# Kernel optimization log

Hardware: AMD Instinct MI355X
Metric: run time of the kernel (lower is better)

## Reference

```python
import jax, jax.numpy as jnp
import numpy as np

N_NODES = 50000
N_EDGES = 800000
IN_F = 128
HID = 64
H1 = 4  # heads layer 1
H2 = 1  # heads layer 2
N_GRAPHS = 32
NEG_SLOPE = 0.2  # PyG GATConv default leaky_relu slope


def _glorot(key, shape):
    fan_in, fan_out = shape[0], shape[-1]
    scale = jnp.sqrt(6.0 / (fan_in + fan_out))
    return jax.random.uniform(key, shape, jnp.float32, -scale, scale)


def setup_inputs() -> dict:
    key = jax.random.key(0)
    ks = jax.random.split(key, 10)
    x = jax.random.normal(ks[0], (N_NODES, IN_F), jnp.float32)
    edge_index = jax.random.randint(ks[1], (2, N_EDGES), 0, N_NODES, jnp.int64)
    batch = jnp.sort(jax.random.randint(ks[2], (N_NODES,), 0, N_GRAPHS, jnp.int64))
    # GATConv layer 1: in 128 -> 4 heads x 64, concat
    W1 = _glorot(ks[3], (IN_F, H1 * HID))
    a_src1 = _glorot(ks[4], (H1, HID))
    a_dst1 = _glorot(ks[5], (H1, HID))
    b1 = jnp.zeros((H1 * HID,), jnp.float32)
    # GATConv layer 2: in 256 -> 1 head x 64
    W2 = _glorot(ks[6], (H1 * HID, H2 * HID))
    a_src2 = _glorot(ks[7], (H2, HID))
    a_dst2 = _glorot(ks[8], (H2, HID))
    b2 = jnp.zeros((H2 * HID,), jnp.float32)
    return {"x": x, "edge_index": edge_index, "batch": batch,
            "W1": W1, "a_src1": a_src1, "a_dst1": a_dst1, "b1": b1,
            "W2": W2, "a_src2": a_src2, "a_dst2": a_dst2, "b2": b2}


def gat_layer(x, src, dst, W, a_src, a_dst, bias, num_nodes):
    """PyG-style GATConv with concat=True output [N, H*C]."""
    H, C = a_src.shape
    h = (x @ W).reshape(num_nodes, H, C)            # [N,H,C]
    alpha_src = jnp.sum(h * a_src[None], axis=-1)   # [N,H]
    alpha_dst = jnp.sum(h * a_dst[None], axis=-1)   # [N,H]
    e = jax.nn.leaky_relu(alpha_src[src] + alpha_dst[dst], NEG_SLOPE)  # [E,H]
    # segment softmax over destination neighborhoods
    m = jax.ops.segment_max(e, dst, num_segments=num_nodes)
    ex = jnp.exp(e - m[dst])
    denom = jax.ops.segment_sum(ex, dst, num_segments=num_nodes)
    alpha = ex / (denom[dst] + 1e-16)               # [E,H]
    out = jax.ops.segment_sum(h[src] * alpha[:, :, None], dst, num_segments=num_nodes)
    return out.reshape(num_nodes, H * C) + bias


def reference(x, edge_index, batch, W1, a_src1, a_dst1, b1, W2, a_src2, a_dst2, b2):
    N = x.shape[0]
    # PyG GATConv adds self-loops by default
    loops = jnp.arange(N, dtype=edge_index.dtype)
    src = jnp.concatenate([edge_index[0], loops])
    dst = jnp.concatenate([edge_index[1], loops])
    h = jax.nn.relu(gat_layer(x, src, dst, W1, a_src1, a_dst1, b1, N))
    h = gat_layer(h, src, dst, W2, a_src2, a_dst2, b2, N)
    # role == 'global': global mean pool over batch ids
    sums = jax.ops.segment_sum(h, batch, num_segments=N_GRAPHS)
    cnt = jax.ops.segment_sum(jnp.ones((N, 1), h.dtype), batch, num_segments=N_GRAPHS)
    return sums / jnp.maximum(cnt, 1.0)
```

## Files before the change

kernel.cpp:

```cpp
#include <hip/hip_runtime.h>
#include <cmath>

#define HID 64
typedef unsigned short ushort_t;
typedef __attribute__((ext_vector_type(8))) short bf16x8;
typedef __attribute__((ext_vector_type(4))) float f32x4;

__device__ inline ushort_t f2b(float f) {
    unsigned u = __float_as_uint(f);
    unsigned r = (u + 0x7fffu + ((u >> 16) & 1u)) >> 16;
    return (ushort_t)r;
}
__device__ inline float b2f(ushort_t b) { return __uint_as_float(((unsigned)b) << 16); }


__global__ void fill_i32(int* __restrict__ p, int v, long n) {
    long i = (long)blockIdx.x * blockDim.x + threadIdx.x;
    long stride = (long)gridDim.x * blockDim.x;
    for (; i < n; i += stride) p[i] = v;
}

__global__ __launch_bounds__(256) void prep_k(const float* __restrict__ W1,
                                              const float* __restrict__ W2,
                                              ushort_t* __restrict__ W1t,
                                              ushort_t* __restrict__ W2t,
                                              const int* __restrict__ batch,
                                              int* __restrict__ cnt_i,
                                              float* __restrict__ outp,
                                              const int* __restrict__ ei,
                                              int* __restrict__ deg,
                                              int N, int E, int NHB) {
    int b = blockIdx.x;
    int t = threadIdx.x;
    if (b < 128) {
        W1t[(size_t)t * 128 + b] = f2b(W1[(size_t)b * 256 + t]);
    } else if (b < 384) {
        int k = b - 128;
        if (t < 64) W2t[(size_t)t * 256 + k] = f2b(W2[(size_t)k * 64 + t]);
    } else if (b == 384) {
        int i = t * 8;
        #pragma unroll
        for (int j = 0; j < 8; ++j) outp[i + j] = 0.f;
    } else if (b < 385 + NHB) {
        __shared__ int lh[32];
        if (t < 32) lh[t] = 0;
        __syncthreads();
        int i = (b - 385) * 256 + t;
        if (i < N) atomicAdd(&lh[batch[i]], 1);
        __syncthreads();
        if (t < 32 && lh[t] > 0) atomicAdd(&cnt_i[t], lh[t]);
    } else {
        int e = (b - 385 - NHB) * 256 + t;
        int T = E + N;
        if (e < T) {
            int d = (e < E) ? ei[E + e] : (e - E);
            atomicAdd(&deg[d], 1);
        }
    }
}


__global__ __launch_bounds__(256) void scan1_k(const int* __restrict__ deg,
                                               int* __restrict__ bsum, int N) {
    int i = blockIdx.x * 256 + threadIdx.x;
    int v = (i < N) ? deg[i] : 0;
    #pragma unroll
    for (int off = 32; off > 0; off >>= 1) v += __shfl_xor(v, off, 64);
    __shared__ int ws[4];
    if ((threadIdx.x & 63) == 0) ws[threadIdx.x >> 6] = v;
    __syncthreads();
    if (threadIdx.x == 0) bsum[blockIdx.x] = ws[0] + ws[1] + ws[2] + ws[3];
}

__global__ __launch_bounds__(256) void scan3_k(const int* __restrict__ deg,
                                               const int* __restrict__ bsum,
                                               int* __restrict__ rowstart, int N, int NB) {
    int t = threadIdx.x;
    int lane = t & 63, wave = t >> 6;
    int pv = (t < NB && t < (int)blockIdx.x) ? bsum[t] : 0;
    #pragma unroll
    for (int off = 32; off > 0; off >>= 1) pv += __shfl_xor(pv, off, 64);
    __shared__ int wsp[4];
    if (lane == 0) wsp[wave] = pv;
    __syncthreads();
    int base = wsp[0] + wsp[1] + wsp[2] + wsp[3];

    int i = blockIdx.x * 256 + t;
    int v = (i < N) ? deg[i] : 0;
    int inc = v;
    #pragma unroll
    for (int off = 1; off < 64; off <<= 1) {
        int u = __shfl_up(inc, off, 64);
        if (lane >= off) inc += u;
    }
    __shared__ int wsum[4];
    if (lane == 63) wsum[wave] = inc;
    __syncthreads();
    int woff = base;
    for (int w = 0; w < wave; ++w) woff += wsum[w];
    int excl = inc - v + woff;
    if (i < N) rowstart[i] = excl;
    if (i == N - 1) rowstart[N] = excl + v;
}

__global__ __launch_bounds__(256) void mega1_k(
        const float* __restrict__ x, const ushort_t* __restrict__ Bt,
        ushort_t* __restrict__ Cb, const float* __restrict__ a_src,
        const float* __restrict__ a_dst, float* __restrict__ os,
        float* __restrict__ od, int M, int NG1,
        const int* __restrict__ ei, int E, int N,
        const int* __restrict__ rowstart, int* __restrict__ cursor,
        int* __restrict__ srcs) {
    __shared__ ushort_t Alds[64][40];
    __shared__ ushort_t Blds[256][40];
    const int tid = threadIdx.x;

    if (blockIdx.x >= NG1) {
        int e = (blockIdx.x - NG1) * 256 + tid;
        int T = E + N;
        if (e < T) {
            int s, d;
            if (e < E) { s = ei[e]; d = ei[E + e]; } else { s = e - E; d = s; }
            int p = atomicAdd(&cursor[d], 1);
            srcs[rowstart[d] + p] = s;
        }
        return;
    }

    const int bm = blockIdx.x * 64;
    const int w = tid >> 6;
    const int l = tid & 63;
    const int lr = l >> 4;
    const int lc = l & 15;
    const int col0 = w * 64;

    f32x4 acc[4][4] = {};

    for (int kk = 0; kk < 4; ++kk) {
        __syncthreads();
        {
            int row = tid >> 2, part = tid & 3;
            int gm = bm + row;
            bf16x8 v = {0, 0, 0, 0, 0, 0, 0, 0};
            if (gm < M) {
                const float* ap = x + (size_t)gm * 128 + kk * 32 + part * 8;
                float4 v0 = *(const float4*)ap;
                float4 v1 = *(const float4*)(ap + 4);
                v[0] = (short)f2b(v0.x); v[1] = (short)f2b(v0.y);
                v[2] = (short)f2b(v0.z); v[3] = (short)f2b(v0.w);
                v[4] = (short)f2b(v1.x); v[5] = (short)f2b(v1.y);
                v[6] = (short)f2b(v1.z); v[7] = (short)f2b(v1.w);
            }
            *(bf16x8*)&Alds[row][part * 8] = v;
        }
        #pragma unroll
        for (int it = 0; it < 4; ++it) {
            int u = tid + it * 256;
            int col = u >> 2, part = u & 3;
            *(bf16x8*)&Blds[col][part * 8] =
                *(const bf16x8*)&Bt[(size_t)col * 128 + kk * 32 + part * 8];
        }
        __syncthreads();

        bf16x8 af[4], bfr[4];
        #pragma unroll
        for (int fr = 0; fr < 4; ++fr)
            af[fr] = *(const bf16x8*)&Alds[fr * 16 + lc][lr * 8];
        #pragma unroll
        for (int fc = 0; fc < 4; ++fc)
            bfr[fc] = *(const bf16x8*)&Blds[col0 + fc * 16 + lc][lr * 8];
        #pragma unroll
        for (int fr = 0; fr < 4; ++fr)
            #pragma unroll
            for (int fc = 0; fc < 4; ++fc)
                acc[fr][fc] = __builtin_amdgcn_mfma_f32_16x16x32_bf16(
                    af[fr], bfr[fc], acc[fr][fc], 0, 0, 0);
    }

    #pragma unroll
    for (int fr = 0; fr < 4; ++fr)
        #pragma unroll
        for (int r = 0; r < 4; ++r) {
            int gm = bm + fr * 16 + lr * 4 + r;
            if (gm >= M) continue;
            #pragma unroll
            for (int fc = 0; fc < 4; ++fc)
                Cb[(size_t)gm * 256 + col0 + fc * 16 + lc] = f2b(acc[fr][fc][r]);
        }

    {
        const int head = w;
        const float* __restrict__ asv = a_src + head * 64;
        const float* __restrict__ adv = a_dst + head * 64;
        #pragma unroll
        for (int fr = 0; fr < 4; ++fr)
            #pragma unroll
            for (int r = 0; r < 4; ++r) {
                float ps = 0.f, pd = 0.f;
                #pragma unroll
                for (int fc = 0; fc < 4; ++fc) {
                    float av = acc[fr][fc][r];
                    ps = fmaf(av, asv[fc * 16 + lc], ps);
                    pd = fmaf(av, adv[fc * 16 + lc], pd);
                }
                #pragma unroll
                for (int off = 1; off < 16; off <<= 1) {
                    ps += __shfl_xor(ps, off, 64);
                    pd += __shfl_xor(pd, off, 64);
                }
                int gm = bm + fr * 16 + lr * 4 + r;
                if (lc == 0 && gm < M) {
                    os[(size_t)gm * 4 + head] = ps;
                    od[(size_t)gm * 4 + head] = pd;
                }
            }
    }
}

template<int WM, int WN, int K, bool B_WHOLE, int AH>
__global__ __launch_bounds__(WM * WN * 64) void gemm_mfma(
        const ushort_t* __restrict__ Ap, const ushort_t* __restrict__ Bt,
        ushort_t* __restrict__ Cb, const float* __restrict__ a_src,
        const float* __restrict__ a_dst, float* __restrict__ os,
        float* __restrict__ od, int M) {
    constexpr int T = WM * WN * 64;
    constexpr int BM = WM * 64;
    constexpr int BN = WN * 64;
    constexpr int BSTR = B_WHOLE ? (K + 8) : 40;

    __shared__ ushort_t Alds[BM][40];
    __shared__ ushort_t Blds[BN][BSTR];

    const int tid = threadIdx.x;
    const int bm = blockIdx.x * BM;
    const int w = tid >> 6;
    const int l = tid & 63;
    const int lr = l >> 4;
    const int lc = l & 15;
    const int row0 = (WM == 1) ? 0 : w * 64;
    const int col0 = (WN == 1) ? 0 : w * 64;

    f32x4 acc[4][4] = {};

    if (B_WHOLE) {
        constexpr int UPR = K / 8;
        for (int u = tid; u < BN * UPR; u += T) {
            int row = u / UPR, j = u % UPR;
            *(bf16x8*)&Blds[row][j * 8] = *(const bf16x8*)&Bt[(size_t)row * K + j * 8];
        }
    }

    for (int kk = 0; kk < K / 32; ++kk) {
        __syncthreads();
        for (int u = tid; u < BM * 4; u += T) {
            int row = u >> 2, part = u & 3;
            int gm = bm + row;
            bf16x8 v = {0, 0, 0, 0, 0, 0, 0, 0};
            if (gm < M)
                v = *(const bf16x8*)(Ap + (size_t)gm * K + kk * 32 + part * 8);
            *(bf16x8*)&Alds[row][part * 8] = v;
        }
        if (!B_WHOLE) {
            for (int u = tid; u < BN * 4; u += T) {
                int col = u >> 2, part = u & 3;
                *(bf16x8*)&Blds[col][part * 8] =
                    *(const bf16x8*)&Bt[(size_t)col * K + kk * 32 + part * 8];
            }
        }
        __syncthreads();

        const int koff = B_WHOLE ? kk * 32 : 0;
        bf16x8 af[4], bfr[4];
        #pragma unroll
        for (int fr = 0; fr < 4; ++fr)
            af[fr] = *(const bf16x8*)&Alds[row0 + fr * 16 + lc][lr * 8];
        #pragma unroll
        for (int fc = 0; fc < 4; ++fc)
            bfr[fc] = *(const bf16x8*)&Blds[col0 + fc * 16 + lc][koff + lr * 8];
        #pragma unroll
        for (int fr = 0; fr < 4; ++fr)
            #pragma unroll
            for (int fc = 0; fc < 4; ++fc)
                acc[fr][fc] = __builtin_amdgcn_mfma_f32_16x16x32_bf16(
                    af[fr], bfr[fc], acc[fr][fc], 0, 0, 0);
    }

    #pragma unroll
    for (int fr = 0; fr < 4; ++fr)
        #pragma unroll
        for (int r = 0; r < 4; ++r) {
            int gm = bm + row0 + fr * 16 + lr * 4 + r;
            if (gm >= M) continue;
            #pragma unroll
            for (int fc = 0; fc < 4; ++fc)
                Cb[(size_t)gm * BN + col0 + fc * 16 + lc] = f2b(acc[fr][fc][r]);
        }

    if (AH > 0) {
        const int head = (WN > 1) ? w : 0;
        const float* __restrict__ asv = a_src + head * 64;
        const float* __restrict__ adv = a_dst + head * 64;
        #pragma unroll
        for (int fr = 0; fr < 4; ++fr)
            #pragma unroll
            for (int r = 0; r < 4; ++r) {
                float ps = 0.f, pd = 0.f;
                #pragma unroll
                for (int fc = 0; fc < 4; ++fc) {
                    float av = acc[fr][fc][r];
                    ps = fmaf(av, asv[fc * 16 + lc], ps);
                    pd = fmaf(av, adv[fc * 16 + lc], pd);
                }
                #pragma unroll
                for (int off = 1; off < 16; off <<= 1) {
                    ps += __shfl_xor(ps, off, 64);
                    pd += __shfl_xor(pd, off, 64);
                }
                int gm = bm + row0 + fr * 16 + lr * 4 + r;
                if (lc == 0 && gm < M) {
                    os[(size_t)gm * AH + head] = ps;
                    od[(size_t)gm * AH + head] = pd;
                }
            }
    }
}

#define MAXD 128
__global__ __launch_bounds__(256) void gat_agg4(const ushort_t* __restrict__ hb,
        const int* __restrict__ rowstart, const int* __restrict__ srcs,
        const float* __restrict__ as, const float* __restrict__ ad,
        const float* __restrict__ bias, ushort_t* __restrict__ outb, int N) {
    __shared__ int ssrc_s[4][MAXD];
    __shared__ float sw_s[4][MAXD][4];
    __shared__ float hstat_s[4][2][4];
    const int wave = threadIdx.x >> 6;
    const int lane = threadIdx.x & 63;
    int d = blockIdx.x * 4 + wave;
    if (d >= N) return;
    int* ssrc = ssrc_s[wave];
    float (*sw)[4] = sw_s[wave];
    int beg = rowstart[d];
    int deg = rowstart[d + 1] - beg;
    int dcap = deg < MAXD ? deg : MAXD;
    for (int i = lane; i < dcap; i += 64) ssrc[i] = srcs[beg + i];

    const int isub = lane >> 2;
    const int hd = lane & 3;
    float adv = ad[d * 4 + hd];
    float vmax = -INFINITY;
    for (int e0 = 0; e0 < deg; e0 += 16) {
        int e = e0 + isub;
        if (e < deg) {
            int s = (e < MAXD) ? ssrc[e] : srcs[beg + e];
            float v = as[s * 4 + hd] + adv;
            v = v > 0.f ? v : 0.2f * v;
            if (e < MAXD) sw[e][hd] = v;
            vmax = fmaxf(vmax, v);
        }
    }
    #pragma unroll
    for (int off = 4; off < 64; off <<= 1) vmax = fmaxf(vmax, __shfl_xor(vmax, off, 64));
    float dsum = 0.f;
    for (int e0 = 0; e0 < deg; e0 += 16) {
        int e = e0 + isub;
        if (e < deg) {
            float v;
            if (e < MAXD) v = sw[e][hd];
            else {
                int s = srcs[beg + e];
                v = as[s * 4 + hd] + adv;
                v = v > 0.f ? v : 0.2f * v;
            }
            float ex = __expf(v - vmax);
            if (e < MAXD) sw[e][hd] = ex;
            dsum += ex;
        }
    }
    #pragma unroll
    for (int off = 4; off < 64; off <<= 1) dsum += __shfl_xor(dsum, off, 64);
    float rden = 1.f / (dsum + 1e-16f);
    for (int e0 = 0; e0 < dcap; e0 += 16) {
        int e = e0 + isub;
        if (e < dcap) sw[e][hd] *= rden;
    }
    if (deg > MAXD && isub == 0) {
        hstat_s[wave][0][hd] = vmax;
        hstat_s[wave][1][hd] = rden;
    }

    const int hd2 = lane >> 4;
    const ushort_t* __restrict__ hrow = hb + (size_t)(lane * 4);
    float a0 = 0.f, a1 = 0.f, a2 = 0.f, a3 = 0.f;
    int e = 0;
    for (; e + 4 <= dcap; e += 4) {
        int s0 = __builtin_amdgcn_readfirstlane(ssrc[e]);
        int s1 = __builtin_amdgcn_readfirstlane(ssrc[e + 1]);
        int s2 = __builtin_amdgcn_readfirstlane(ssrc[e + 2]);
        int s3 = __builtin_amdgcn_readfirstlane(ssrc[e + 3]);
        ushort4 g0 = *(const ushort4*)(hrow + (size_t)s0 * 256);
        ushort4 g1 = *(const ushort4*)(hrow + (size_t)s1 * 256);
        ushort4 g2 = *(const ushort4*)(hrow + (size_t)s2 * 256);
        ushort4 g3 = *(const ushort4*)(hrow + (size_t)s3 * 256);
        float w0 = sw[e][hd2], w1 = sw[e + 1][hd2];
        float w2 = sw[e + 2][hd2], w3 = sw[e + 3][hd2];
        a0 = fmaf(b2f(g0.x), w0, a0); a1 = fmaf(b2f(g0.y), w0, a1);
        a2 = fmaf(b2f(g0.z), w0, a2); a3 = fmaf(b2f(g0.w), w0, a3);
        a0 = fmaf(b2f(g1.x), w1, a0); a1 = fmaf(b2f(g1.y), w1, a1);
        a2 = fmaf(b2f(g1.z), w1, a2); a3 = fmaf(b2f(g1.w), w1, a3);
        a0 = fmaf(b2f(g2.x), w2, a0); a1 = fmaf(b2f(g2.y), w2, a1);
        a2 = fmaf(b2f(g2.z), w2, a2); a3 = fmaf(b2f(g2.w), w2, a3);
        a0 = fmaf(b2f(g3.x), w3, a0); a1 = fmaf(b2f(g3.y), w3, a1);
        a2 = fmaf(b2f(g3.z), w3, a2); a3 = fmaf(b2f(g3.w), w3, a3);
    }
    for (; e < dcap; ++e) {
        int s = __builtin_amdgcn_readfirstlane(ssrc[e]);
        float w = sw[e][hd2];
        ushort4 g = *(const ushort4*)(hrow + (size_t)s * 256);
        a0 = fmaf(b2f(g.x), w, a0); a1 = fmaf(b2f(g.y), w, a1);
        a2 = fmaf(b2f(g.z), w, a2); a3 = fmaf(b2f(g.w), w, a3);
    }
    if (deg > MAXD) {
        float vm2 = hstat_s[wave][0][hd2];
        float rd2 = hstat_s[wave][1][hd2];
        float adv2 = ad[d * 4 + hd2];
        for (int j = MAXD; j < deg; ++j) {
            int s = srcs[beg + j];
            float v = as[s * 4 + hd2] + adv2;
            v = v > 0.f ? v : 0.2f * v;
            float w = __expf(v - vm2) * rd2;
            ushort4 g = *(const ushort4*)(hrow + (size_t)s * 256);
            a0 = fmaf(b2f(g.x), w, a0); a1 = fmaf(b2f(g.y), w, a1);
            a2 = fmaf(b2f(g.z), w, a2); a3 = fmaf(b2f(g.w), w, a3);
        }
    }
    int cb = lane * 4;
    ushort4 ov;
    ov.x = f2b(fmaxf(a0 + bias[cb + 0], 0.f));
    ov.y = f2b(fmaxf(a1 + bias[cb + 1], 0.f));
    ov.z = f2b(fmaxf(a2 + bias[cb + 2], 0.f));
    ov.w = f2b(fmaxf(a3 + bias[cb + 3], 0.f));
    *(ushort4*)&outb[(size_t)d * 256 + cb] = ov;
}

__global__ __launch_bounds__(256) void gat_agg1(const ushort_t* __restrict__ hb,
        const int* __restrict__ rowstart, const int* __restrict__ srcs,
        const float* __restrict__ as, const float* __restrict__ ad,
        const float* __restrict__ bias, const int* __restrict__ batch,
        const int* __restrict__ cnt_i, float* __restrict__ outp, int N) {
    __shared__ int ssrc_s[4][MAXD];
    __shared__ float sw_s[4][MAXD];
    __shared__ float prow[4][64];
    __shared__ int gws[4];
    const int wave = threadIdx.x >> 6;
    const int lane = threadIdx.x & 63;
    int d = blockIdx.x * 4 + wave;
    bool active = d < N;
    if (active) {
        int* ssrc = ssrc_s[wave];
        float* sw = sw_s[wave];
        int beg = rowstart[d];
        int deg = rowstart[d + 1] - beg;
        int dcap = deg < MAXD ? deg : MAXD;
        for (int i = lane; i < dcap; i += 64) ssrc[i] = srcs[beg + i];

        float adv = ad[d];
        float vmax = -INFINITY;
        for (int e0 = 0; e0 < deg; e0 += 64) {
            int e = e0 + lane;
            if (e < deg) {
                int s = (e < MAXD) ? ssrc[e] : srcs[beg + e];
                float v = as[s] + adv;
                v = v > 0.f ? v : 0.2f * v;
                if (e < MAXD) sw[e] = v;
                vmax = fmaxf(vmax, v);
            }
        }
        #pragma unroll
        for (int off = 1; off < 64; off <<= 1) vmax = fmaxf(vmax, __shfl_xor(vmax, off, 64));
        float dsum = 0.f;
        for (int e0 = 0; e0 < deg; e0 += 64) {
            int e = e0 + lane;
            if (e < deg) {
                float v;
                if (e < MAXD) v = sw[e];
                else {
                    int s = srcs[beg + e];
                    v = as[s] + adv;
                    v = v > 0.f ? v : 0.2f * v;
                }
                float ex = __expf(v - vmax);
                if (e < MAXD) sw[e] = ex;
                dsum += ex;
            }
        }
        #pragma unroll
        for (int off = 1; off < 64; off <<= 1) dsum += __shfl_xor(dsum, off, 64);
        float rden = 1.f / (dsum + 1e-16f);
        for (int e0 = 0; e0 < dcap; e0 += 64) {
            int e = e0 + lane;
            if (e < dcap) sw[e] *= rden;
        }

        const int esub = lane >> 4;
        const int cg = lane & 15;
        const ushort_t* __restrict__ hrow = hb + (size_t)(cg * 4);
        float a0 = 0.f, a1 = 0.f, a2 = 0.f, a3 = 0.f;
        int e0 = 0;
        for (; e0 + 8 <= dcap; e0 += 8) {
            int eA = e0 + esub, eB = e0 + esub + 4;
            int sA = ssrc[eA], sB = ssrc[eB];
            float wA = sw[eA], wB = sw[eB];
            ushort4 gA = *(const ushort4*)(hrow + (size_t)sA * 64);
            ushort4 gB = *(const ushort4*)(hrow + (size_t)sB * 64);
            a0 = fmaf(b2f(gA.x), wA, a0); a1 = fmaf(b2f(gA.y), wA, a1);
            a2 = fmaf(b2f(gA.z), wA, a2); a3 = fmaf(b2f(gA.w), wA, a3);
            a0 = fmaf(b2f(gB.x), wB, a0); a1 = fmaf(b2f(gB.y), wB, a1);
            a2 = fmaf(b2f(gB.z), wB, a2); a3 = fmaf(b2f(gB.w), wB, a3);
        }
        for (; e0 < dcap; e0 += 4) {
            int e = e0 + esub;
            if (e < dcap) {
                int s = ssrc[e];
                float w = sw[e];
                ushort4 g = *(const ushort4*)(hrow + (size_t)s * 64);
                a0 = fmaf(b2f(g.x), w, a0); a1 = fmaf(b2f(g.y), w, a1);
                a2 = fmaf(b2f(g.z), w, a2); a3 = fmaf(b2f(g.w), w, a3);
            }
        }
        for (int j = MAXD + esub; j < deg; j += 4) {
            int s = srcs[beg + j];
            float v = as[s] + adv;
            v = v > 0.f ? v : 0.2f * v;
            float w = __expf(v - vmax) * rden;
            ushort4 g = *(const ushort4*)(hrow + (size_t)s * 64);
            a0 = fmaf(b2f(g.x), w, a0); a1 = fmaf(b2f(g.y), w, a1);
            a2 = fmaf(b2f(g.z), w, a2); a3 = fmaf(b2f(g.w), w, a3);
        }
        a0 += __shfl_xor(a0, 16, 64); a0 += __shfl_xor(a0, 32, 64);
        a1 += __shfl_xor(a1, 16, 64); a1 += __shfl_xor(a1, 32, 64);
        a2 += __shfl_xor(a2, 16, 64); a2 += __shfl_xor(a2, 32, 64);
        a3 += __shfl_xor(a3, 16, 64); a3 += __shfl_xor(a3, 32, 64);
        int g = batch[d];
        if (esub == 0) {
            float cntf = fmaxf((float)cnt_i[g], 1.f);
            float rc = 1.f / cntf;
            int cb = cg * 4;
            float4 o;
            o.x = (a0 + bias[cb + 0]) * rc;
            o.y = (a1 + bias[cb + 1]) * rc;
            o.z = (a2 + bias[cb + 2]) * rc;
            o.w = (a3 + bias[cb + 3]) * rc;
            *(float4*)&prow[wave][cb] = o;
        }
        if (lane == 0) gws[wave] = g;
    } else {
        if (lane == 0) gws[wave] = -1;
    }
    __syncthreads();
    if (threadIdx.x < 64) {
        int t = threadIdx.x;
        int g0 = gws[0];
        if (g0 >= 0 && gws[1] == g0 && gws[2] == g0 && gws[3] == g0) {
            atomicAdd(&outp[g0 * 64 + t],
                      prow[0][t] + prow[1][t] + prow[2][t] + prow[3][t]);
        } else {
            #pragma unroll
            for (int w2 = 0; w2 < 4; ++w2)
                if (gws[w2] >= 0) atomicAdd(&outp[gws[w2] * 64 + t], prow[w2][t]);
        }
    }
}


extern "C" void kernel_launch(void* const* d_in, const int* in_sizes, int n_in,
                              void* d_out, int out_size, void* d_ws, size_t ws_size,
                              hipStream_t stream) {
    const float* x      = (const float*)d_in[0];
    const int*   ei     = (const int*)d_in[1];
    const int*   batch  = (const int*)d_in[2];
    const float* W1     = (const float*)d_in[3];
    const float* a_src1 = (const float*)d_in[4];
    const float* a_dst1 = (const float*)d_in[5];
    const float* b1     = (const float*)d_in[6];
    const float* W2     = (const float*)d_in[7];
    const float* a_src2 = (const float*)d_in[8];
    const float* a_dst2 = (const float*)d_in[9];
    const float* b2     = (const float*)d_in[10];
    float* out = (float*)d_out;

    const int N = in_sizes[0] / 128;
    const int E = in_sizes[1] / 2;
    const int F1 = 256;
    const int F2 = 64;
    const int T = E + N;
    const int NB = (N + 255) / 256;
    const int NCB = (T + 255) / 256;
    const int NG1 = (N + 63) / 64;

    float* ws = (float*)d_ws;
    size_t o = 0;
    ushort_t* h1b   = (ushort_t*)(ws + o); o += (size_t)N * F1 / 2;
    ushort_t* out1b = (ushort_t*)(ws + o); o += (size_t)N * F1 / 2;
    ushort_t* h2b   = (ushort_t*)(ws + o); o += (size_t)N * F2 / 2;
    float* asrc1 = ws + o; o += (size_t)N * 4;
    float* adst1 = ws + o; o += (size_t)N * 4;
    float* asrc2 = ws + o; o += (size_t)N;
    float* adst2 = ws + o; o += (size_t)N;
    ushort_t* W1t = (ushort_t*)(ws + o); o += 256 * 128 / 2;
    ushort_t* W2t = (ushort_t*)(ws + o); o += 64 * 256 / 2;
    int* ib = (int*)(ws + o);
    size_t io = 0;
    int* deg      = ib + io; io += N;
    int* cursor   = ib + io; io += N;
    int* cnt_i    = ib + io; io += 32;
    int* rowstart = ib + io; io += N + 1;
    int* bsum     = ib + io; io += NB;
    int* srcs     = ib + io; io += T;
    (void)ws_size; (void)n_in; (void)out_size;

    fill_i32<<<256, 256, 0, stream>>>(deg, 0, 2L * N + 32);
    prep_k<<<385 + NB + NCB, 256, 0, stream>>>(W1, W2, W1t, W2t, batch, cnt_i, out,
                                               ei, deg, N, E, NB);

    scan1_k<<<NB, 256, 0, stream>>>(deg, bsum, N);
    scan3_k<<<NB, 256, 0, stream>>>(deg, bsum, rowstart, N, NB);

    mega1_k<<<NG1 + NCB, 256, 0, stream>>>(x, W1t, h1b, a_src1, a_dst1,
                                           asrc1, adst1, N, NG1,
                                           ei, E, N, rowstart, cursor, srcs);

    gat_agg4<<<(N + 3) / 4, 256, 0, stream>>>(h1b, rowstart, srcs, asrc1, adst1, b1, out1b, N);

    gemm_mfma<2, 1, 256, true, 1><<<(N + 127) / 128, 128, 0, stream>>>(
        out1b, W2t, h2b, a_src2, a_dst2, asrc2, adst2, N);
    gat_agg1<<<(N + 3) / 4, 256, 0, stream>>>(h2b, rowstart, srcs, asrc2, adst2, b2,
                                              batch, cnt_i, out, N);
}
```

Measured before the change: 237.7 us.

## Store layer-1 features head-major and gather per head with edge-split lanes

The layer-1 GEMM output is now written in a head-major layout ([head][node][64]) instead of interleaved rows of 256. The aggregation kernel loops over the four heads. In each head, 16 lanes cover the 64 channels and 4 lane groups take different edges, and their partial sums are combined with cross-lane shuffles. The aim is for each head's gather to touch a contiguous 128-byte row and to get more independent loads in flight per wave. The cost is four passes over the edge list, extra shuffle reductions, and only a quarter of the lanes doing the final stores.

```diff
diff --git a/kernel.cpp b/kernel.cpp
--- a/kernel.cpp
+++ b/kernel.cpp
@@ -177,6 +177,7 @@
                     af[fr], bfr[fc], acc[fr][fc], 0, 0, 0);
     }
 
+    ushort_t* __restrict__ Ch = Cb + (size_t)w * M * 64;
     #pragma unroll
     for (int fr = 0; fr < 4; ++fr)
         #pragma unroll
@@ -185,7 +186,7 @@
             if (gm >= M) continue;
             #pragma unroll
             for (int fc = 0; fc < 4; ++fc)
-                Cb[(size_t)gm * 256 + col0 + fc * 16 + lc] = f2b(acc[fr][fc][r]);
+                Ch[(size_t)gm * 64 + fc * 16 + lc] = f2b(acc[fr][fc][r]);
         }
 
     {
@@ -383,63 +384,67 @@
         int e = e0 + isub;
         if (e < dcap) sw[e][hd] *= rden;
     }
-    if (deg > MAXD && isub == 0) {
+    if (isub == 0) {
         hstat_s[wave][0][hd] = vmax;
         hstat_s[wave][1][hd] = rden;
     }
 
-    const int hd2 = lane >> 4;
-    const ushort_t* __restrict__ hrow = hb + (size_t)(lane * 4);
-    float a0 = 0.f, a1 = 0.f, a2 = 0.f, a3 = 0.f;
-    int e = 0;
-    for (; e + 4 <= dcap; e += 4) {
-        int s0 = __builtin_amdgcn_readfirstlane(ssrc[e]);
-        int s1 = __builtin_amdgcn_readfirstlane(ssrc[e + 1]);
-        int s2 = __builtin_amdgcn_readfirstlane(ssrc[e + 2]);
-        int s3 = __builtin_amdgcn_readfirstlane(ssrc[e + 3]);
-        ushort4 g0 = *(const ushort4*)(hrow + (size_t)s0 * 256);
-        ushort4 g1 = *(const ushort4*)(hrow + (size_t)s1 * 256);
-        ushort4 g2 = *(const ushort4*)(hrow + (size_t)s2 * 256);
-        ushort4 g3 = *(const ushort4*)(hrow + (size_t)s3 * 256);
-        float w0 = sw[e][hd2], w1 = sw[e + 1][hd2];
-        float w2 = sw[e + 2][hd2], w3 = sw[e + 3][hd2];
-        a0 = fmaf(b2f(g0.x), w0, a0); a1 = fmaf(b2f(g0.y), w0, a1);
-        a2 = fmaf(b2f(g0.z), w0, a2); a3 = fmaf(b2f(g0.w), w0, a3);
-        a0 = fmaf(b2f(g1.x), w1, a0); a1 = fmaf(b2f(g1.y), w1, a1);
-        a2 = fmaf(b2f(g1.z), w1, a2); a3 = fmaf(b2f(g1.w), w1, a3);
-        a0 = fmaf(b2f(g2.x), w2, a0); a1 = fmaf(b2f(g2.y), w2, a1);
-        a2 = fmaf(b2f(g2.z), w2, a2); a3 = fmaf(b2f(g2.w), w2, a3);
-        a0 = fmaf(b2f(g3.x), w3, a0); a1 = fmaf(b2f(g3.y), w3, a1);
-        a2 = fmaf(b2f(g3.z), w3, a2); a3 = fmaf(b2f(g3.w), w3, a3);
-    }
-    for (; e < dcap; ++e) {
-        int s = __builtin_amdgcn_readfirstlane(ssrc[e]);
-        float w = sw[e][hd2];
-        ushort4 g = *(const ushort4*)(hrow + (size_t)s * 256);
-        a0 = fmaf(b2f(g.x), w, a0); a1 = fmaf(b2f(g.y), w, a1);
-        a2 = fmaf(b2f(g.z), w, a2); a3 = fmaf(b2f(g.w), w, a3);
-    }
-    if (deg > MAXD) {
-        float vm2 = hstat_s[wave][0][hd2];
-        float rd2 = hstat_s[wave][1][hd2];
-        float adv2 = ad[d * 4 + hd2];
-        for (int j = MAXD; j < deg; ++j) {
-            int s = srcs[beg + j];
-            float v = as[s * 4 + hd2] + adv2;
-            v = v > 0.f ? v : 0.2f * v;
-            float w = __expf(v - vm2) * rd2;
-            ushort4 g = *(const ushort4*)(hrow + (size_t)s * 256);
-            a0 = fmaf(b2f(g.x), w, a0); a1 = fmaf(b2f(g.y), w, a1);
-            a2 = fmaf(b2f(g.z), w, a2); a3 = fmaf(b2f(g.w), w, a3);
-        }
-    }
-    int cb = lane * 4;
-    ushort4 ov;
-    ov.x = f2b(fmaxf(a0 + bias[cb + 0], 0.f));
-    ov.y = f2b(fmaxf(a1 + bias[cb + 1], 0.f));
-    ov.z = f2b(fmaxf(a2 + bias[cb + 2], 0.f));
-    ov.w = f2b(fmaxf(a3 + bias[cb + 3], 0.f));
-    *(ushort4*)&outb[(size_t)d * 256 + cb] = ov;
+    const int esub = lane >> 4;
+    const int cg = lane & 15;
+    #pragma unroll
+    for (int h = 0; h < 4; ++h) {
+        const ushort_t* __restrict__ hrow = hb + (size_t)h * N * 64 + cg * 4;
+        float a0 = 0.f, a1 = 0.f, a2 = 0.f, a3 = 0.f;
+        int e0 = 0;
+        for (; e0 + 8 <= dcap; e0 += 8) {
+            int eA = e0 + esub, eB = e0 + esub + 4;
+            int sA = ssrc[eA], sB = ssrc[eB];
+            float wA = sw[eA][h], wB = sw[eB][h];
+            ushort4 gA = *(const ushort4*)(hrow + (size_t)sA * 64);
+            ushort4 gB = *(const ushort4*)(hrow + (size_t)sB * 64);
+            a0 = fmaf(b2f(gA.x), wA, a0); a1 = fmaf(b2f(gA.y), wA, a1);
+            a2 = fmaf(b2f(gA.z), wA, a2); a3 = fmaf(b2f(gA.w), wA, a3);
+            a0 = fmaf(b2f(gB.x), wB, a0); a1 = fmaf(b2f(gB.y), wB, a1);
+            a2 = fmaf(b2f(gB.z), wB, a2); a3 = fmaf(b2f(gB.w), wB, a3);
+        }
+        for (; e0 < dcap; e0 += 4) {
+            int e = e0 + esub;
+            if (e < dcap) {
+                int s = ssrc[e];
+                float w = sw[e][h];
+                ushort4 g = *(const ushort4*)(hrow + (size_t)s * 64);
+                a0 = fmaf(b2f(g.x), w, a0); a1 = fmaf(b2f(g.y), w, a1);
+                a2 = fmaf(b2f(g.z), w, a2); a3 = fmaf(b2f(g.w), w, a3);
+            }
+        }
+        if (deg > MAXD) {
+            float vm2 = hstat_s[wave][0][h];
+            float rd2 = hstat_s[wave][1][h];
+            float adv2 = ad[d * 4 + h];
+            for (int j = MAXD + esub; j < deg; j += 4) {
+                int s = srcs[beg + j];
+                float v = as[s * 4 + h] + adv2;
+                v = v > 0.f ? v : 0.2f * v;
+                float w = __expf(v - vm2) * rd2;
+                ushort4 g = *(const ushort4*)(hrow + (size_t)s * 64);
+                a0 = fmaf(b2f(g.x), w, a0); a1 = fmaf(b2f(g.y), w, a1);
+                a2 = fmaf(b2f(g.z), w, a2); a3 = fmaf(b2f(g.w), w, a3);
+            }
+        }
+        a0 += __shfl_xor(a0, 16, 64); a0 += __shfl_xor(a0, 32, 64);
+        a1 += __shfl_xor(a1, 16, 64); a1 += __shfl_xor(a1, 32, 64);
+        a2 += __shfl_xor(a2, 16, 64); a2 += __shfl_xor(a2, 32, 64);
+        a3 += __shfl_xor(a3, 16, 64); a3 += __shfl_xor(a3, 32, 64);
+        if (esub == 0) {
+            int cb = h * 64 + cg * 4;
+            ushort4 ov;
+            ov.x = f2b(fmaxf(a0 + bias[cb + 0], 0.f));
+            ov.y = f2b(fmaxf(a1 + bias[cb + 1], 0.f));
+            ov.z = f2b(fmaxf(a2 + bias[cb + 2], 0.f));
+            ov.w = f2b(fmaxf(a3 + bias[cb + 3], 0.f));
+            *(ushort4*)&outb[(size_t)d * 256 + cb] = ov;
+        }
+    }
 }
 
 __global__ __launch_bounds__(256) void gat_agg1(const ushort_t* __restrict__ hb,
```

New measurement: 251.2 us. 1.06x slower.

## Merge scan kernels and widen layer-1 GEMM blocks to 128 rows

Applied to the files above, without the earlier changes.

The two-pass block scan is replaced by a single kernel in which each block re-sums all preceding degree entries to get its base offset. This removes one launch and the block-sum buffer, but adds redundant prefix reads that grow with the block index. The fused layer-1 GEMM and CSR-fill kernel now runs 512 threads per block over 128 rows. Eight waves split into two row halves times four heads, so each staged W1 tile is reused across twice as many rows. The edge-scatter blocks are resized to match.

```diff
diff --git a/kernel.cpp b/kernel.cpp
--- a/kernel.cpp
+++ b/kernel.cpp
@@ -59,25 +59,13 @@
     }
 }
 
-
-__global__ __launch_bounds__(256) void scan1_k(const int* __restrict__ deg,
-                                               int* __restrict__ bsum, int N) {
-    int i = blockIdx.x * 256 + threadIdx.x;
-    int v = (i < N) ? deg[i] : 0;
-    #pragma unroll
-    for (int off = 32; off > 0; off >>= 1) v += __shfl_xor(v, off, 64);
-    __shared__ int ws[4];
-    if ((threadIdx.x & 63) == 0) ws[threadIdx.x >> 6] = v;
-    __syncthreads();
-    if (threadIdx.x == 0) bsum[blockIdx.x] = ws[0] + ws[1] + ws[2] + ws[3];
-}
-
-__global__ __launch_bounds__(256) void scan3_k(const int* __restrict__ deg,
-                                               const int* __restrict__ bsum,
-                                               int* __restrict__ rowstart, int N, int NB) {
+__global__ __launch_bounds__(256) void scan_k(const int* __restrict__ deg,
+                                              int* __restrict__ rowstart, int N) {
     int t = threadIdx.x;
     int lane = t & 63, wave = t >> 6;
-    int pv = (t < NB && t < (int)blockIdx.x) ? bsum[t] : 0;
+    int limit = blockIdx.x * 256;
+    int pv = 0;
+    for (int i = t; i < limit; i += 256) pv += deg[i];
     #pragma unroll
     for (int off = 32; off > 0; off >>= 1) pv += __shfl_xor(pv, off, 64);
     __shared__ int wsp[4];
@@ -85,7 +73,7 @@
     __syncthreads();
     int base = wsp[0] + wsp[1] + wsp[2] + wsp[3];
 
-    int i = blockIdx.x * 256 + t;
+    int i = limit + t;
     int v = (i < N) ? deg[i] : 0;
     int inc = v;
     #pragma unroll
@@ -103,7 +91,7 @@
     if (i == N - 1) rowstart[N] = excl + v;
 }
 
-__global__ __launch_bounds__(256) void mega1_k(
+__global__ __launch_bounds__(512) void mega1_k(
         const float* __restrict__ x, const ushort_t* __restrict__ Bt,
         ushort_t* __restrict__ Cb, const float* __restrict__ a_src,
         const float* __restrict__ a_dst, float* __restrict__ os,
@@ -111,12 +99,12 @@
         const int* __restrict__ ei, int E, int N,
         const int* __restrict__ rowstart, int* __restrict__ cursor,
         int* __restrict__ srcs) {
-    __shared__ ushort_t Alds[64][40];
+    __shared__ ushort_t Alds[128][40];
     __shared__ ushort_t Blds[256][40];
     const int tid = threadIdx.x;
 
     if (blockIdx.x >= NG1) {
-        int e = (blockIdx.x - NG1) * 256 + tid;
+        int e = (blockIdx.x - NG1) * 512 + tid;
         int T = E + N;
         if (e < T) {
             int s, d;
@@ -127,12 +115,15 @@
         return;
     }
 
-    const int bm = blockIdx.x * 64;
+    const int bm = blockIdx.x * 128;
     const int w = tid >> 6;
     const int l = tid & 63;
     const int lr = l >> 4;
     const int lc = l & 15;
-    const int col0 = w * 64;
+    const int rh = w >> 2;
+    const int head = w & 3;
+    const int row0 = rh * 64;
+    const int col0 = head * 64;
 
     f32x4 acc[4][4] = {};
 
@@ -154,8 +145,8 @@
             *(bf16x8*)&Alds[row][part * 8] = v;
         }
         #pragma unroll
-        for (int it = 0; it < 4; ++it) {
-            int u = tid + it * 256;
+        for (int it = 0; it < 2; ++it) {
+            int u = tid + it * 512;
             int col = u >> 2, part = u & 3;
             *(bf16x8*)&Blds[col][part * 8] =
                 *(const bf16x8*)&Bt[(size_t)col * 128 + kk * 32 + part * 8];
@@ -165,7 +156,7 @@
         bf16x8 af[4], bfr[4];
         #pragma unroll
         for (int fr = 0; fr < 4; ++fr)
-            af[fr] = *(const bf16x8*)&Alds[fr * 16 + lc][lr * 8];
+            af[fr] = *(const bf16x8*)&Alds[row0 + fr * 16 + lc][lr * 8];
         #pragma unroll
         for (int fc = 0; fc < 4; ++fc)
             bfr[fc] = *(const bf16x8*)&Blds[col0 + fc * 16 + lc][lr * 8];
@@ -181,7 +172,7 @@
     for (int fr = 0; fr < 4; ++fr)
         #pragma unroll
         for (int r = 0; r < 4; ++r) {
-            int gm = bm + fr * 16 + lr * 4 + r;
+            int gm = bm + row0 + fr * 16 + lr * 4 + r;
             if (gm >= M) continue;
             #pragma unroll
             for (int fc = 0; fc < 4; ++fc)
@@ -189,7 +180,6 @@
         }
 
     {
-        const int head = w;
         const float* __restrict__ asv = a_src + head * 64;
         const float* __restrict__ adv = a_dst + head * 64;
         #pragma unroll
@@ -208,7 +198,7 @@
                     ps += __shfl_xor(ps, off, 64);
                     pd += __shfl_xor(pd, off, 64);
                 }
-                int gm = bm + fr * 16 + lr * 4 + r;
+                int gm = bm + row0 + fr * 16 + lr * 4 + r;
                 if (lc == 0 && gm < M) {
                     os[(size_t)gm * 4 + head] = ps;
                     od[(size_t)gm * 4 + head] = pd;
@@ -595,7 +585,8 @@
     const int T = E + N;
     const int NB = (N + 255) / 256;
     const int NCB = (T + 255) / 256;
-    const int NG1 = (N + 63) / 64;
+    const int NSB = (T + 511) / 512;
+    const int NG1 = (N + 127) / 128;
 
     float* ws = (float*)d_ws;
     size_t o = 0;
@@ -614,7 +605,6 @@
     int* cursor   = ib + io; io += N;
     int* cnt_i    = ib + io; io += 32;
     int* rowstart = ib + io; io += N + 1;
-    int* bsum     = ib + io; io += NB;
     int* srcs     = ib + io; io += T;
     (void)ws_size; (void)n_in; (void)out_size;
 
@@ -622,10 +612,9 @@
     prep_k<<<385 + NB + NCB, 256, 0, stream>>>(W1, W2, W1t, W2t, batch, cnt_i, out,
                                                ei, deg, N, E, NB);
 
-    scan1_k<<<NB, 256, 0, stream>>>(deg, bsum, N);
-    scan3_k<<<NB, 256, 0, stream>>>(deg, bsum, rowstart, N, NB);
-
-    mega1_k<<<NG1 + NCB, 256, 0, stream>>>(x, W1t, h1b, a_src1, a_dst1,
+    scan_k<<<NB, 256, 0, stream>>>(deg, rowstart, N);
+
+    mega1_k<<<NG1 + NSB, 512, 0, stream>>>(x, W1t, h1b, a_src1, a_dst1,
                                            asrc1, adst1, N, NG1,
                                            ei, E, N, rowstart, cursor, srcs);
 
```

Measured after the change: 253.8 us. 6.8% more time.
